# Kernel optimization log

Hardware: AMD Instinct MI355X
Metric: run time of the kernel (lower is better)

## Reference

```python
import jax, jax.numpy as jnp
import numpy as np

B, N, DIM = 64, 784, 256
N1, N2, HS, WS, M, D = 1, 4, 28, 7, 8, 2  # x_windows, y_windows, H_sp, W_sp, num_heads, d
HW = HS * WS                              # 196 tokens per window
C = DIM // M                              # 32 channels per head


def setup_inputs() -> dict:
    key = jax.random.key(0)
    ks = jax.random.split(key, 5)
    x = jax.random.normal(ks[0], (B, N, DIM), dtype=jnp.float32)
    Wc = jax.random.normal(ks[1], (DIM, M * D), dtype=jnp.float32) * 0.02
    bc = jax.random.normal(ks[2], (M * D,), dtype=jnp.float32) * 0.02
    Wg = jax.random.normal(ks[3], (HW * D, HW * HW), dtype=jnp.float32) * 0.02
    bg = jax.random.normal(ks[4], (HW * HW,), dtype=jnp.float32) * 0.02
    return {"x": x, "Wc": Wc, "bc": bc, "Wg": Wg, "bg": bg}


def reference(x, Wc, bc, Wg, bg):
    b = x.shape[0]
    # compress: B N C -> B N (m d)
    w = x @ Wc + bc
    # rearrange 'b (n1 h n2 w) (m d) -> b (n1 n2 m) (h w d)'
    w = w.reshape(b, N1, HS, N2, WS, M, D)
    w = w.transpose(0, 1, 3, 5, 2, 4, 6).reshape(b, N1 * N2 * M, HW * D)
    # generate per-window mixing weights: B Nw (HW*HW)
    w = w @ Wg + bg
    w = w.reshape(b, N1 * N2 * M, HW, HW)
    # softmax over dim=-2 (the (h1 w1) source axis)
    w = jax.nn.softmax(w, axis=-2)
    # rearrange x: 'b (n1 h1 n2 w1) (m c) -> b (n1 n2 m) c (h1 w1)'
    xv = x.reshape(b, N1, HS, N2, WS, M, C)
    xv = xv.transpose(0, 1, 3, 5, 6, 2, 4).reshape(b, N1 * N2 * M, C, HW)
    # windowed mixing matmul: (b, Nw, C, HW) @ (b, Nw, HW, HW)
    out = jnp.matmul(xv, w)
    # rearrange back: 'b (n1 n2 m) c (h2 w2) -> b (n1 h2 n2 w2) (m c)'
    out = out.reshape(b, N1, N2, M, C, HS, WS)
    out = out.transpose(0, 1, 5, 2, 6, 3, 4).reshape(b, N1 * HS * N2 * WS, M * C)
    return out
```

## Files before the change

### kernel.cpp

```cpp
#include <hip/hip_runtime.h>
#include <hip/hip_bf16.h>
#include <stdint.h>
#include <stddef.h>

#define NB    64
#define NTOK  784
#define DIMC  256
#define NN2   4
#define NM    8
#define NHW   196
#define NWIN  32
#define NROWS 2048
#define NK    392
#define NKP   448
#define NBIG  38416
#define NIP   200
#define STROW 39200
#define STROW2 39232
#define NPT   39424
#define NTT   307
#define PTS   232

typedef __attribute__((ext_vector_type(4))) float f32x4;
typedef __attribute__((ext_vector_type(8))) short bf16x8;

static __device__ __forceinline__ float bf2f(unsigned short u) {
  union { unsigned int i; float f; } v; v.i = ((unsigned int)u) << 16; return v.f;
}
static __device__ __forceinline__ unsigned short f2bf(float f) {
  union { float f; unsigned int i; } v; v.f = f;
  unsigned int r = v.i + 0x7fffu + ((v.i >> 16) & 1u);
  return (unsigned short)(r >> 16);
}

__global__ __launch_bounds__(256) void k_compress(
    const float* __restrict__ x, const float* __restrict__ Wc,
    const float* __restrict__ bc, unsigned short* __restrict__ Abf) {
  __shared__ float wcs[16 * 256];
  __shared__ float bcs[16];
  const int tid = threadIdx.x;
  const int b  = blockIdx.x / NN2;
  const int n2 = blockIdx.x % NN2;
  for (int idx = tid; idx < 4096; idx += 256) {
    int c = idx >> 4, md = idx & 15;
    wcs[md * 256 + c] = Wc[idx];
  }
  if (tid < 16) bcs[tid] = bc[tid];
  __syncthreads();
  if (tid < NHW) {
    const int h = tid / 7, wcol = tid % 7;
    const int t = h * 28 + n2 * 7 + wcol;
    const float* xp = x + ((size_t)b * NTOK + t) * DIMC;
    float acc[16];
    #pragma unroll
    for (int md = 0; md < 16; ++md) acc[md] = bcs[md];
    for (int c = 0; c < 256; c += 4) {
      const f32x4 xv = *(const f32x4*)(xp + c);
      #pragma unroll
      for (int md = 0; md < 16; ++md) {
        const f32x4 wv = *(const f32x4*)(wcs + md * 256 + c);
        acc[md] += xv[0]*wv[0] + xv[1]*wv[1] + xv[2]*wv[2] + xv[3]*wv[3];
      }
    }
    #pragma unroll
    for (int md = 0; md < 16; ++md) {
      const int m = md >> 1, d = md & 1;
      const int r = b * NWIN + n2 * NM + m;
      Abf[(size_t)r * NKP + tid * 2 + d] = f2bf(acc[md]);
    }
  }
  for (int e = tid; e < NM * (NKP - NK); e += 256) {
    const int m = e / (NKP - NK);
    const int k = NK + (e % (NKP - NK));
    const int r = b * NWIN + n2 * NM + m;
    Abf[(size_t)r * NKP + k] = (k == NK) ? (unsigned short)0x3F80 : 0;
  }
}

__global__ __launch_bounds__(256) void k_wgt(
    const float* __restrict__ Wg, const float* __restrict__ bg,
    unsigned short* __restrict__ Wgbt) {
  __shared__ float tile[64][65];
  const int bid = blockIdx.x;
  const int n0 = (bid % 601) * 64;
  const int k0 = (bid / 601) * 64;
  const int tid = threadIdx.x;
  for (int idx = tid; idx < 4096; idx += 256) {
    const int kk = idx >> 6, nn = idx & 63;
    const int k = k0 + kk, n = n0 + nn;
    float v = 0.f;
    if (n < NBIG) {
      if (k < NK) v = Wg[(size_t)k * NBIG + n];
      else if (k == NK) v = bg[n];
    }
    tile[nn][kk] = v;
  }
  __syncthreads();
  for (int idx = tid; idx < 512; idx += 256) {
    const int nn = idx >> 3, gg = idx & 7;
    const int n = n0 + nn;
    if (n < NBIG) {
      const int i = n / NHW, j = n - (n / NHW) * NHW;
      const int np = j * NIP + i;
      unsigned short u8[8];
      #pragma unroll
      for (int e = 0; e < 8; ++e) u8[e] = f2bf(tile[nn][gg * 8 + e]);
      *(uint4*)&Wgbt[(size_t)np * NKP + k0 + gg * 8] = *(const uint4*)u8;
    }
  }
}

__global__ __launch_bounds__(256) void k_zero(unsigned short* __restrict__ Wgbt) {
  const int bid = blockIdx.x;
  int np;
  if (bid < 784) { const int j = bid >> 2, i = 196 + (bid & 3); np = j * NIP + i; }
  else           { np = STROW + (bid - 784); }
  unsigned int* p = (unsigned int*)(Wgbt + (size_t)np * NKP);
  if (threadIdx.x < 224) p[threadIdx.x] = 0u;
}

__global__ __launch_bounds__(256) void k_gemm(
    const unsigned short* __restrict__ A,
    const unsigned short* __restrict__ Bt,
    unsigned short* __restrict__ E, int mtiles) {
  __shared__ __align__(128) short smem[32768];
  const int tid = threadIdx.x;
  const int w = tid >> 6, lane = tid & 63;
  const int nwg = gridDim.x;
  const int q = nwg >> 3, rr = nwg & 7;
  const int xcd = blockIdx.x & 7, pos = blockIdx.x >> 3;
  const int wg = (xcd < rr ? xcd * (q + 1) : rr * (q + 1) + (xcd - rr) * q) + pos;
  const int nt = wg / mtiles, mt = wg % mtiles;
  const int m0 = mt * 128, n0 = nt * 128;
  const int wm = (w >> 1) * 64, wn = (w & 1) * 64;
  const int lrow = lane >> 3;
  const int lcolsw = ((lane & 7) ^ lrow) * 8;

  const unsigned short* Arow = A  + (size_t)(m0 + w * 32 + lrow) * NKP + lcolsw;
  const unsigned short* Brow = Bt + (size_t)(n0 + w * 32 + lrow) * NKP + lcolsw;

  auto stage = [&](int kt, int buf) {
    #pragma unroll
    for (int is = 0; is < 4; ++is) {
      const int gg = w * 4 + is;
      __builtin_amdgcn_global_load_lds(
          (const __attribute__((address_space(1))) void*)(Arow + (size_t)is * 8 * NKP + kt),
          (__attribute__((address_space(3))) void*)((char*)smem + buf * 16384 + gg * 1024), 16, 0, 0);
      __builtin_amdgcn_global_load_lds(
          (const __attribute__((address_space(1))) void*)(Brow + (size_t)is * 8 * NKP + kt),
          (__attribute__((address_space(3))) void*)((char*)smem + 32768 + buf * 16384 + gg * 1024), 16, 0, 0);
    }
  };

  f32x4 acc[4][4] = {};
  stage(0, 0);
  __syncthreads();
  const int lq = lane >> 4;
  const int lx = (lane & 7);
  for (int t = 0; t < 7; ++t) {
    const int buf = t & 1;
    if (t < 6) stage((t + 1) * 64, buf ^ 1);
    const short* ab = smem + buf * 8192;
    const short* bb = smem + 16384 + buf * 8192;
    #pragma unroll
    for (int kk = 0; kk < 2; ++kk) {
      bf16x8 af[4], bfr[4];
      #pragma unroll
      for (int i = 0; i < 4; ++i) {
        const int row = wm + i * 16 + (lane & 15);
        const int slot = ((kk * 4 + lq) ^ lx) * 8;
        af[i]  = *(const bf16x8*)(ab + row * 64 + slot);
        const int rowb = wn + i * 16 + (lane & 15);
        bfr[i] = *(const bf16x8*)(bb + rowb * 64 + slot);
      }
      #pragma unroll
      for (int mi = 0; mi < 4; ++mi)
        #pragma unroll
        for (int ni = 0; ni < 4; ++ni)
          acc[mi][ni] = __builtin_amdgcn_mfma_f32_16x16x32_bf16(af[mi], bfr[ni], acc[mi][ni], 0, 0, 0);
    }
    __syncthreads();
  }

  const int cq = lane >> 4, cr = lane & 15;
  #pragma unroll
  for (int mi = 0; mi < 4; ++mi)
    #pragma unroll
    for (int ni = 0; ni < 4; ++ni)
      #pragma unroll
      for (int e = 0; e < 4; ++e) {
        const int rl = wm + mi * 16 + cq * 4 + e;
        const int cl = wn + ni * 16 + cr;
        smem[rl * 132 + cl] = (short)f2bf(__expf(acc[mi][ni][e]));
      }
  __syncthreads();
  for (int idx = tid; idx < 2048; idx += 256) {
    const int rl = idx >> 4, seg = idx & 15;
    const int col0 = n0 + seg * 8;
    if (col0 < STROW2) {
      const uint4 v = *(const uint4*)&smem[rl * 132 + seg * 8];
      *(uint4*)&E[(size_t)(m0 + rl) * STROW2 + col0] = v;
    }
  }
}

__global__ __launch_bounds__(512) void k_mix(
    const unsigned short* __restrict__ E, const float* __restrict__ x,
    float* __restrict__ out, int row0) {
  __shared__ unsigned short Elds[22528];
  __shared__ unsigned short xvT[32 * PTS];
  const int tid = threadIdx.x, w = tid >> 6, lane = tid & 63;
  const int row = blockIdx.x >> 1, jh = blockIdx.x & 1;
  const int r = row0 + row;
  const int b = r >> 5, win = r & 31, n2 = win >> 3, m = win & 7;

  const unsigned short* Eb = E + (size_t)row * STROW2;
  const int g0 = jh ? 2800 : 0;
  const int nch = jh ? 33 : 44;
  for (int ch = w; ch < nch; ch += 8) {
    const int gr = g0 + ch * 64 + lane;
    if (gr < 4904)
      __builtin_amdgcn_global_load_lds(
          (const __attribute__((address_space(1))) void*)(Eb + (size_t)gr * 8),
          (__attribute__((address_space(3))) void*)((char*)Elds + ch * 1024), 16, 0, 0);
  }

  for (int idx = tid; idx < 1568; idx += 512) {
    const int i = idx >> 3, c4 = (idx & 7) * 4;
    const int t = (i / 7) * 28 + n2 * 7 + (i % 7);
    const f32x4 v = *(const f32x4*)(x + ((size_t)b * NTOK + t) * DIMC + m * 32 + c4);
    xvT[(c4 + 0) * PTS + i] = f2bf(v[0]);
    xvT[(c4 + 1) * PTS + i] = f2bf(v[1]);
    xvT[(c4 + 2) * PTS + i] = f2bf(v[2]);
    xvT[(c4 + 3) * PTS + i] = f2bf(v[3]);
  }
  for (int idx = tid; idx < 32 * (PTS - NHW); idx += 512) {
    const int c = idx / (PTS - NHW), i = NHW + idx % (PTS - NHW);
    xvT[c * PTS + i] = 0;
  }
  __syncthreads();

  bf16x8 bfr[2][7];
  #pragma unroll
  for (int ct = 0; ct < 2; ++ct)
    #pragma unroll
    for (int kk = 0; kk < 7; ++kk)
      bfr[ct][kk] = *(const bf16x8*)&xvT[(ct * 16 + (lane & 15)) * PTS + kk * 32 + (lane >> 4) * 8];
  const bool den = (lane & 15) == 0;
  bf16x8 oneA, oneB;
  #pragma unroll
  for (int e = 0; e < 8; ++e) {
    oneA[e] = den ? (short)0x3F80 : (short)0;
    const int i6 = 192 + (lane >> 4) * 8 + e;
    oneB[e] = (den && i6 < NHW) ? (short)0x3F80 : (short)0;
  }

  const int jt0 = jh ? 7 : 0;
  const int jtend = jh ? 13 : 7;
  for (int jt = jt0 + w; jt < jtend; jt += 8) {
    const int jA = jt * 16 + (lane & 15);
    const int jAc = (jA < NHW) ? jA : NHW - 1;
    const unsigned short* rp = Elds + jAc * NIP - jh * 22400 + (lane >> 4) * 8;
    bf16x8 af[7];
    #pragma unroll
    for (int kk = 0; kk < 7; ++kk) af[kk] = *(const bf16x8*)(rp + kk * 32);
    f32x4 a0 = {0.f,0.f,0.f,0.f}, a1 = {0.f,0.f,0.f,0.f}, ad = {0.f,0.f,0.f,0.f};
    #pragma unroll
    for (int kk = 0; kk < 7; ++kk) {
      a0 = __builtin_amdgcn_mfma_f32_16x16x32_bf16(af[kk], bfr[0][kk], a0, 0, 0, 0);
      a1 = __builtin_amdgcn_mfma_f32_16x16x32_bf16(af[kk], bfr[1][kk], a1, 0, 0, 0);
      ad = __builtin_amdgcn_mfma_f32_16x16x32_bf16(af[kk], (kk < 6) ? oneA : oneB, ad, 0, 0, 0);
    }
    const int c = lane & 15;
    #pragma unroll
    for (int e = 0; e < 4; ++e) {
      const int j = jt * 16 + (lane >> 4) * 4 + e;
      const float dv = __shfl(ad[e], lane & 48);
      if (j < NHW) {
        const float inv = 1.f / dv;
        const int t2 = (j / 7) * 28 + n2 * 7 + (j % 7);
        float* op = out + ((size_t)b * NTOK + t2) * DIMC + m * 32;
        op[c] = a0[e] * inv;
        op[c + 16] = a1[e] * inv;
      }
    }
  }
}

extern "C" void kernel_launch(void* const* d_in, const int* in_sizes, int n_in,
                              void* d_out, int out_size, void* d_ws, size_t ws_size,
                              hipStream_t stream) {
  const float* x  = (const float*)d_in[0];
  const float* Wc = (const float*)d_in[1];
  const float* bc = (const float*)d_in[2];
  const float* Wg = (const float*)d_in[3];
  const float* bg = (const float*)d_in[4];
  float* out = (float*)d_out;

  char* ws = (char*)d_ws;
  const size_t wgbt_bytes = (size_t)NPT * NKP * 2;
  const size_t a_bytes    = (size_t)NROWS * NKP * 2;
  unsigned short* Wgbt = (unsigned short*)ws;
  unsigned short* Abf  = (unsigned short*)(ws + wgbt_bytes);
  unsigned short* E    = (unsigned short*)(ws + wgbt_bytes + a_bytes);
  const size_t fixed = wgbt_bytes + a_bytes;
  const size_t srow_bytes = (size_t)STROW2 * 2;

  size_t avail = (ws_size > fixed) ? (ws_size - fixed) : 0;
  int rows_chunk = (int)(avail / srow_bytes);
  rows_chunk = (rows_chunk / 128) * 128;
  if (rows_chunk > NROWS) rows_chunk = NROWS;
  if (rows_chunk < 128)  rows_chunk = 128;

  hipLaunchKernelGGL(k_compress, dim3(NB * NN2), dim3(256), 0, stream, x, Wc, bc, Abf);
  hipLaunchKernelGGL(k_wgt, dim3(601 * 7), dim3(256), 0, stream, Wg, bg, Wgbt);
  hipLaunchKernelGGL(k_zero, dim3(1008), dim3(256), 0, stream, Wgbt);
  for (int row0 = 0; row0 < NROWS; row0 += rows_chunk) {
    int rc = NROWS - row0; if (rc > rows_chunk) rc = rows_chunk;
    hipLaunchKernelGGL(k_gemm, dim3((rc / 128) * NTT), dim3(256), 0, stream,
                       Abf + (size_t)row0 * NKP, Wgbt, E, rc / 128);
    hipLaunchKernelGGL(k_mix, dim3(rc * 2), dim3(512), 0, stream, E, x, out, row0);
  }
}
```

Before: 216.0 us.

## Enlarge GEMM tile to 256x256 with 512 threads and finer waitcnt pipelining

The exp-GEMM block tile grows from 128x128 to 256x256, with 8 waves each computing a 64x128 sub-tile. Four waves stage A and four stage B into a 128KB double-buffered LDS. The per-iteration __syncthreads are replaced by explicit vmcnt waits and raw barriers so the next stage's loads overlap compute. The epilogue writes the exponentiated tile in two 128-row halves through LDS. The aim is more operand reuse per LDS byte and fewer workgroups, at the cost of higher register and LDS pressure and lower occupancy.

```diff
diff --git a/kernel.cpp b/kernel.cpp
--- a/kernel.cpp
+++ b/kernel.cpp
@@ -18,7 +18,7 @@
 #define STROW 39200
 #define STROW2 39232
 #define NPT   39424
-#define NTT   307
+#define NTT   154
 #define PTS   232
 
 typedef __attribute__((ext_vector_type(4))) float f32x4;
@@ -119,11 +119,11 @@
   if (threadIdx.x < 224) p[threadIdx.x] = 0u;
 }
 
-__global__ __launch_bounds__(256) void k_gemm(
+__global__ __launch_bounds__(512, 2) void k_gemm(
     const unsigned short* __restrict__ A,
     const unsigned short* __restrict__ Bt,
     unsigned short* __restrict__ E, int mtiles) {
-  __shared__ __align__(128) short smem[32768];
+  __shared__ __align__(128) short smem[65536];
   const int tid = threadIdx.x;
   const int w = tid >> 6, lane = tid & 63;
   const int nwg = gridDim.x;
@@ -131,75 +131,92 @@
   const int xcd = blockIdx.x & 7, pos = blockIdx.x >> 3;
   const int wg = (xcd < rr ? xcd * (q + 1) : rr * (q + 1) + (xcd - rr) * q) + pos;
   const int nt = wg / mtiles, mt = wg % mtiles;
-  const int m0 = mt * 128, n0 = nt * 128;
-  const int wm = (w >> 1) * 64, wn = (w & 1) * 64;
-  const int lrow = lane >> 3;
-  const int lcolsw = ((lane & 7) ^ lrow) * 8;
-
-  const unsigned short* Arow = A  + (size_t)(m0 + w * 32 + lrow) * NKP + lcolsw;
-  const unsigned short* Brow = Bt + (size_t)(n0 + w * 32 + lrow) * NKP + lcolsw;
+  const int m0 = mt * 256, n0 = nt * 256;
+  const int lrow = lane >> 3, lgran = lane & 7;
+  const int srcg = (lgran ^ lrow) * 8;
+
+  const unsigned short* srow = (w < 4)
+      ? A  + (size_t)(m0 + w * 64 + lrow) * NKP + srcg
+      : Bt + (size_t)(n0 + (w - 4) * 64 + lrow) * NKP + srcg;
+  const int dstb0 = ((w < 4) ? 0 : 32768) + (w & 3) * 8192;
 
   auto stage = [&](int kt, int buf) {
     #pragma unroll
-    for (int is = 0; is < 4; ++is) {
-      const int gg = w * 4 + is;
+    for (int is = 0; is < 8; ++is) {
       __builtin_amdgcn_global_load_lds(
-          (const __attribute__((address_space(1))) void*)(Arow + (size_t)is * 8 * NKP + kt),
-          (__attribute__((address_space(3))) void*)((char*)smem + buf * 16384 + gg * 1024), 16, 0, 0);
-      __builtin_amdgcn_global_load_lds(
-          (const __attribute__((address_space(1))) void*)(Brow + (size_t)is * 8 * NKP + kt),
-          (__attribute__((address_space(3))) void*)((char*)smem + 32768 + buf * 16384 + gg * 1024), 16, 0, 0);
+          (const __attribute__((address_space(1))) void*)(srow + (size_t)is * 8 * NKP + kt),
+          (__attribute__((address_space(3))) void*)((char*)smem + buf * 65536 + dstb0 + is * 1024),
+          16, 0, 0);
     }
   };
 
-  f32x4 acc[4][4] = {};
+  const int wm0 = (w >> 1) * 64;
+  const int wn0 = (w & 1) * 128;
+  const int lq = lane >> 4, lx = lane & 7, cr = lane & 15;
+  f32x4 acc[4][8] = {};
+
   stage(0, 0);
-  __syncthreads();
-  const int lq = lane >> 4;
-  const int lx = (lane & 7);
+  #pragma unroll
   for (int t = 0; t < 7; ++t) {
-    const int buf = t & 1;
-    if (t < 6) stage((t + 1) * 64, buf ^ 1);
-    const short* ab = smem + buf * 8192;
-    const short* bb = smem + 16384 + buf * 8192;
+    if (t < 6) {
+      stage((t + 1) * 64, (t + 1) & 1);
+      asm volatile("s_waitcnt vmcnt(8)" ::: "memory");
+    } else {
+      asm volatile("s_waitcnt vmcnt(0)" ::: "memory");
+    }
+    __builtin_amdgcn_s_barrier();
+    asm volatile("" ::: "memory");
+    const short* ab = smem + (t & 1) * 32768;
+    const short* bb = ab + 16384;
     #pragma unroll
     for (int kk = 0; kk < 2; ++kk) {
-      bf16x8 af[4], bfr[4];
-      #pragma unroll
-      for (int i = 0; i < 4; ++i) {
-        const int row = wm + i * 16 + (lane & 15);
-        const int slot = ((kk * 4 + lq) ^ lx) * 8;
-        af[i]  = *(const bf16x8*)(ab + row * 64 + slot);
-        const int rowb = wn + i * 16 + (lane & 15);
-        bfr[i] = *(const bf16x8*)(bb + rowb * 64 + slot);
-      }
+      const int slot = ((kk * 4 + lq) ^ lx) * 8;
+      bf16x8 af[4], bfr[8];
+      #pragma unroll
+      for (int mi = 0; mi < 4; ++mi)
+        af[mi] = *(const bf16x8*)(ab + (wm0 + mi * 16 + cr) * 64 + slot);
+      #pragma unroll
+      for (int ni = 0; ni < 8; ++ni)
+        bfr[ni] = *(const bf16x8*)(bb + (wn0 + ni * 16 + cr) * 64 + slot);
       #pragma unroll
       for (int mi = 0; mi < 4; ++mi)
         #pragma unroll
-        for (int ni = 0; ni < 4; ++ni)
+        for (int ni = 0; ni < 8; ++ni)
           acc[mi][ni] = __builtin_amdgcn_mfma_f32_16x16x32_bf16(af[mi], bfr[ni], acc[mi][ni], 0, 0, 0);
     }
-    __syncthreads();
-  }
-
-  const int cq = lane >> 4, cr = lane & 15;
+    asm volatile("" ::: "memory");
+    __builtin_amdgcn_s_barrier();
+  }
+
   #pragma unroll
-  for (int mi = 0; mi < 4; ++mi)
-    #pragma unroll
-    for (int ni = 0; ni < 4; ++ni)
-      #pragma unroll
-      for (int e = 0; e < 4; ++e) {
-        const int rl = wm + mi * 16 + cq * 4 + e;
-        const int cl = wn + ni * 16 + cr;
-        smem[rl * 132 + cl] = (short)f2bf(__expf(acc[mi][ni][e]));
+  for (int h = 0; h < 2; ++h) {
+    if (h) {
+      asm volatile("" ::: "memory");
+      __builtin_amdgcn_s_barrier();
+      asm volatile("" ::: "memory");
+    }
+    if ((w >> 2) == h) {
+      #pragma unroll
+      for (int mi = 0; mi < 4; ++mi)
+        #pragma unroll
+        for (int ni = 0; ni < 8; ++ni)
+          #pragma unroll
+          for (int e = 0; e < 4; ++e) {
+            const int rl = wm0 - h * 128 + mi * 16 + lq * 4 + e;
+            const int cl = wn0 + ni * 16 + cr;
+            smem[rl * 264 + cl] = (short)f2bf(__expf(acc[mi][ni][e]));
+          }
+    }
+    asm volatile("" ::: "memory");
+    __builtin_amdgcn_s_barrier();
+    asm volatile("" ::: "memory");
+    for (int g = tid; g < 4096; g += 512) {
+      const int rl = g >> 5, seg = g & 31;
+      const int col0 = n0 + seg * 8;
+      if (col0 < STROW2) {
+        const uint4 v = *(const uint4*)&smem[rl * 264 + seg * 8];
+        *(uint4*)&E[(size_t)(m0 + h * 128 + rl) * STROW2 + col0] = v;
       }
-  __syncthreads();
-  for (int idx = tid; idx < 2048; idx += 256) {
-    const int rl = idx >> 4, seg = idx & 15;
-    const int col0 = n0 + seg * 8;
-    if (col0 < STROW2) {
-      const uint4 v = *(const uint4*)&smem[rl * 132 + seg * 8];
-      *(uint4*)&E[(size_t)(m0 + rl) * STROW2 + col0] = v;
     }
   }
 }
@@ -308,17 +325,17 @@
 
   size_t avail = (ws_size > fixed) ? (ws_size - fixed) : 0;
   int rows_chunk = (int)(avail / srow_bytes);
-  rows_chunk = (rows_chunk / 128) * 128;
+  rows_chunk = (rows_chunk / 256) * 256;
   if (rows_chunk > NROWS) rows_chunk = NROWS;
-  if (rows_chunk < 128)  rows_chunk = 128;
+  if (rows_chunk < 256)  rows_chunk = 256;
 
   hipLaunchKernelGGL(k_compress, dim3(NB * NN2), dim3(256), 0, stream, x, Wc, bc, Abf);
   hipLaunchKernelGGL(k_wgt, dim3(601 * 7), dim3(256), 0, stream, Wg, bg, Wgbt);
   hipLaunchKernelGGL(k_zero, dim3(1008), dim3(256), 0, stream, Wgbt);
   for (int row0 = 0; row0 < NROWS; row0 += rows_chunk) {
     int rc = NROWS - row0; if (rc > rows_chunk) rc = rows_chunk;
-    hipLaunchKernelGGL(k_gemm, dim3((rc / 128) * NTT), dim3(256), 0, stream,
-                       Abf + (size_t)row0 * NKP, Wgbt, E, rc / 128);
+    hipLaunchKernelGGL(k_gemm, dim3((rc / 256) * NTT), dim3(512), 0, stream,
+                       Abf + (size_t)row0 * NKP, Wgbt, E, rc / 256);
     hipLaunchKernelGGL(k_mix, dim3(rc * 2), dim3(512), 0, stream, E, x, out, row0);
   }
 }
```

Result: slower. 221.5 us (+2.5%).
